# Performance work log

Measured on AMD Instinct MI355X. Metric: run time of the kernel, lower is better.

Reference implementation:

```python
import jax, jax.numpy as jnp
import numpy as np

# dims
E, NB = 16, 4            # encoders, blocks per encoder
B, T = 4, 16             # batch, seq_len
DIN, DM, H = 32, 512, 512  # input dim, block state dim, block hidden
FH = 2048                # per-encoder FFNN hidden
ENC_OUT = 512            # per-encoder output dim
DEC_H, DEC_O, DEC_NH = 2048, 1024, 4  # decoder hidden, output, num hidden layers (num_layers=6 -> in + 4 hidden + out)


def setup_inputs() -> dict:
    key = jax.random.key(0)
    ks = iter(jax.random.split(key, 64))
    s = 0.02
    def p(*shape):
        return jax.random.normal(next(ks), shape, dtype=jnp.float32) * s
    inp = {
        "x": jax.random.normal(next(ks), (B, T, DIN), dtype=jnp.float32),
        # block 0 of each encoder: input = cat[x(32), state(512)] -> 544
        "e0_W0": p(E, DIN + DM, H), "e0_b0": jnp.zeros((E, H), jnp.float32),
        "e0_W1": p(E, H, H),        "e0_b1": jnp.zeros((E, H), jnp.float32),
        "e0_W2": p(E, H, DM),       "e0_b2": jnp.zeros((E, DM), jnp.float32),
        # blocks 1..3: input = cat[prev_state_out(512), state(512)] -> 1024
        "er_W0": p(NB - 1, E, 2 * DM, H), "er_b0": jnp.zeros((NB - 1, E, H), jnp.float32),
        "er_W1": p(NB - 1, E, H, H),      "er_b1": jnp.zeros((NB - 1, E, H), jnp.float32),
        "er_W2": p(NB - 1, E, H, DM),     "er_b2": jnp.zeros((NB - 1, E, DM), jnp.float32),
        # per-encoder FFNN over cat of 4 block states (4*512=2048)
        "ff_W0": p(E, NB * DM, FH), "ff_b0": jnp.zeros((E, FH), jnp.float32),
        "ff_W1": p(E, FH, ENC_OUT), "ff_b1": jnp.zeros((E, ENC_OUT), jnp.float32),
        # decoder recurrent cell: input = cat[16*512, dec_state(1024)] = 9216
        "dec_W0": p(E * ENC_OUT + DEC_O, DEC_H), "dec_b0": jnp.zeros((DEC_H,), jnp.float32),
        "dec_Wh": p(DEC_NH, DEC_H, DEC_H),       "dec_bh": jnp.zeros((DEC_NH, DEC_H), jnp.float32),
        "dec_Wo": p(DEC_H, DEC_O),               "dec_bo": jnp.zeros((DEC_O,), jnp.float32),
    }
    return inp


def reference(x, e0_W0, e0_b0, e0_W1, e0_b1, e0_W2, e0_b2,
              er_W0, er_b0, er_W1, er_b1, er_W2, er_b2,
              ff_W0, ff_b0, ff_W1, ff_b1,
              dec_W0, dec_b0, dec_Wh, dec_bh, dec_Wo, dec_bo):
    Bsz = x.shape[0]

    def elin(z, W, b):  # per-encoder batched linear: (E,B,i) @ (E,i,o)
        return jnp.einsum('ebi,eio->ebo', z, W) + b[:, None, :]

    def step(carry, x_t):
        enc_s, dec_s = carry  # enc_s: (NB,E,B,DM); dec_s: (B,DEC_O)
        xin = jnp.broadcast_to(x_t[None], (E, Bsz, DIN))
        # block 0 cell
        z = jnp.concatenate([xin, enc_s[0]], -1)
        h = jax.nn.gelu(elin(z, e0_W0, e0_b0))
        h = jax.nn.gelu(elin(h, e0_W1, e0_b1))
        s = jnp.tanh(elin(h, e0_W2, e0_b2))
        new_s = [s]
        # blocks 1..3 (fixed small structural loop)
        for r in range(NB - 1):
            z = jnp.concatenate([s, enc_s[r + 1]], -1)
            h = jax.nn.gelu(elin(z, er_W0[r], er_b0[r]))
            h = jax.nn.gelu(elin(h, er_W1[r], er_b1[r]))
            s = jnp.tanh(elin(h, er_W2[r], er_b2[r]))
            new_s.append(s)
        new_enc = jnp.stack(new_s, 0)
        # per-encoder FFNN over concatenated block states
        cat = jnp.concatenate(new_s, -1)  # (E,B,NB*DM)
        out = jax.nn.gelu(elin(cat, ff_W0, ff_b0))
        out = elin(out, ff_W1, ff_b1)     # (E,B,ENC_OUT)
        # decoder recurrent cell over cat of all encoder outputs
        dec_in = jnp.transpose(out, (1, 0, 2)).reshape(Bsz, E * ENC_OUT)
        z = jnp.concatenate([dec_in, dec_s], -1)
        h = jax.nn.gelu(z @ dec_W0 + dec_b0)
        for i in range(DEC_NH):
            h = jax.nn.gelu(h @ dec_Wh[i] + dec_bh[i])
        new_dec = jnp.tanh(h @ dec_Wo + dec_bo)
        return (new_enc, new_dec), new_dec

    enc0 = jnp.zeros((NB, E, Bsz, DM), x.dtype)
    dec0 = jnp.zeros((Bsz, DEC_O), x.dtype)
    _, ys = jax.lax.scan(step, (enc0, dec0), jnp.transpose(x, (1, 0, 2)))
    return jnp.transpose(ys, (1, 0, 2))  # (B,T,DEC_O)
```

## Files before the change

### kernel.cpp

```cpp
#include <hip/hip_runtime.h>
#include <math.h>
#include <stdint.h>

#define AG __HIP_MEMORY_SCOPE_AGENT
typedef unsigned long long ull;

__device__ __forceinline__ float ld4(const float* p) {
  return __hip_atomic_load(p, __ATOMIC_RELAXED, AG);
}
__device__ __forceinline__ void st4(float* p, float v) {
  __hip_atomic_store(p, v, __ATOMIC_RELAXED, AG);
}
__device__ __forceinline__ ull ld8(const float* p) {
  return __hip_atomic_load((const ull*)p, __ATOMIC_RELAXED, AG);
}
__device__ __forceinline__ void fence_vm() {
  asm volatile("s_waitcnt vmcnt(0)" ::: "memory");
}
__device__ __forceinline__ void waitge(unsigned* c, unsigned tgt) {
  if (threadIdx.x == 0) {
    while ((int)(__hip_atomic_load(c, __ATOMIC_RELAXED, AG) - tgt) < 0)
      __builtin_amdgcn_s_sleep(1);
  }
  __syncthreads();
}
__device__ __forceinline__ void wait_epoch(unsigned* line, unsigned epoch) {
  if (threadIdx.x == 0) {
    while ((int)(__hip_atomic_load(line, __ATOMIC_RELAXED, AG) - epoch) < 0)
      __builtin_amdgcn_s_sleep(1);
  }
  __syncthreads();
}
__device__ __forceinline__ void wr2(float* d, ull v) {
  d[0] = __uint_as_float((unsigned)v);
  d[1] = __uint_as_float((unsigned)(v >> 32));
}
__device__ __forceinline__ float act_apply(int act, float v) {
  if (act == 0) {
    float v3 = v * v * v;
    return 0.5f * v * (1.0f + tanhf(0.7978845608028654f * (v + 0.044715f * v3)));
  }
  if (act == 1) return tanhf(v);
  return v;
}

__device__ __forceinline__ void stage_signal(unsigned* stageCnt, unsigned bcT,
                                             unsigned* flag, unsigned epoch,
                                             unsigned* sflag) {
  const int tid = threadIdx.x;
  if (tid == 0) {
    unsigned old = __hip_atomic_fetch_add(stageCnt, 1u, __ATOMIC_RELAXED, AG);
    *sflag = (bcT && old == bcT - 1) ? 1u : 0u;
  }
  __syncthreads();
  if (*sflag) {
    if (tid < 64) __hip_atomic_store(flag + tid * 16, epoch, __ATOMIC_RELAXED, AG);
  }
  __syncthreads();
}

template <int KC, class ZL8, class ST>
__device__ void p4(const float* __restrict__ W, int ldw, const float* __restrict__ bias,
                   int c0, int k0, int chunk, int act, int kc, unsigned kcTgt,
                   unsigned* kcCnt, float* part,
                   unsigned* stageCnt, unsigned bcT, unsigned* flag, unsigned epoch,
                   float* lds, unsigned* sflag, ZL8&& zl8, ST&& store) {
  const int tid = threadIdx.x;
  __syncthreads();
  const int cp = chunk >> 1;
  for (int i = tid; i < 4 * cp; i += 256) {
    int b = i / cp, kp = i - b * cp;
    wr2(&lds[b * chunk + 2 * kp], zl8(b, (k0 >> 1) + kp));
  }
  __syncthreads();
  const int q = tid >> 6, lane = tid & 63;
  const int kg = lane >> 4, j4 = lane & 15;
  const int sub = chunk >> 2;
  const int nk = sub >> 2;
  float acc[4][4];
#pragma unroll
  for (int r = 0; r < 4; ++r)
#pragma unroll
    for (int c = 0; c < 4; ++c) acc[r][c] = 0.f;
  const float* wp = W + (size_t)(k0 + q * sub + kg) * ldw + (c0 + 4 * j4);
  const float* zq = lds + q * sub + kg;
#pragma unroll 16
  for (int kk = 0; kk < nk; ++kk) {
    float4 w4 = *(const float4*)(wp + (size_t)(4 * kk) * ldw);
    float z0 = zq[4 * kk];
    float z1 = zq[chunk + 4 * kk];
    float z2 = zq[2 * chunk + 4 * kk];
    float z3 = zq[3 * chunk + 4 * kk];
    acc[0][0] = fmaf(z0, w4.x, acc[0][0]); acc[0][1] = fmaf(z0, w4.y, acc[0][1]);
    acc[0][2] = fmaf(z0, w4.z, acc[0][2]); acc[0][3] = fmaf(z0, w4.w, acc[0][3]);
    acc[1][0] = fmaf(z1, w4.x, acc[1][0]); acc[1][1] = fmaf(z1, w4.y, acc[1][1]);
    acc[1][2] = fmaf(z1, w4.z, acc[1][2]); acc[1][3] = fmaf(z1, w4.w, acc[1][3]);
    acc[2][0] = fmaf(z2, w4.x, acc[2][0]); acc[2][1] = fmaf(z2, w4.y, acc[2][1]);
    acc[2][2] = fmaf(z2, w4.z, acc[2][2]); acc[2][3] = fmaf(z2, w4.w, acc[2][3]);
    acc[3][0] = fmaf(z3, w4.x, acc[3][0]); acc[3][1] = fmaf(z3, w4.y, acc[3][1]);
    acc[3][2] = fmaf(z3, w4.z, acc[3][2]); acc[3][3] = fmaf(z3, w4.w, acc[3][3]);
  }
  __syncthreads();
  float* red = lds;
  float* myred = red + (q * 4 + kg) * 256 + j4 * 16;
#pragma unroll
  for (int b = 0; b < 4; ++b) {
    float4 v4;
    v4.x = acc[b][0]; v4.y = acc[b][1]; v4.z = acc[b][2]; v4.w = acc[b][3];
    *(float4*)(myred + b * 4) = v4;
  }
  __syncthreads();
  const int j4o = tid >> 4, bb = (tid >> 2) & 3, cc = tid & 3;
  const int oj = 4 * j4o + cc;
  float v = 0.f;
#pragma unroll
  for (int g = 0; g < 16; ++g) v += red[g * 256 + j4o * 16 + bb * 4 + cc];
  if constexpr (KC == 1) {
    if (bias) v += bias[c0 + oj];
    v = act_apply(act, v);
    store(bb, c0 + oj, v);
    fence_vm();
    __syncthreads();
    stage_signal(stageCnt, bcT, flag, epoch, sflag);
  } else {
    st4(&part[kc * 256 + oj * 4 + bb], v);
    fence_vm();
    __syncthreads();
    if (tid == 0) {
      unsigned old = __hip_atomic_fetch_add(kcCnt, 1u, __ATOMIC_RELAXED, AG);
      *sflag = (old == kcTgt - 1) ? 1u : 0u;
    }
    __syncthreads();
    if (*sflag) {
      float s = 0.f;
#pragma unroll
      for (int g = 0; g < KC; ++g) s += ld4(&part[g * 256 + oj * 4 + bb]);
      if (bias) s += bias[c0 + oj];
      s = act_apply(act, s);
      store(bb, c0 + oj, s);
      fence_vm();
      __syncthreads();
      stage_signal(stageCnt, bcT, flag, epoch, sflag);
    }
  }
  __syncthreads();
}

template <int KC, class ZL8, class ST>
__device__ void p64(const float* __restrict__ W, int ldw, const float* __restrict__ bias,
                    int c0, int k0, int k1, int act, int kc, unsigned kcTgt,
                    unsigned* kcCnt, float* part,
                    unsigned* stageCnt, unsigned bcT, unsigned* flag, unsigned epoch,
                    float* lds, unsigned* sflag, ZL8&& zl8, ST&& store) {
  const int tid = threadIdx.x;
  const int tj = tid & 15, tr = tid >> 4;
  float acc[4][4];
#pragma unroll
  for (int r = 0; r < 4; ++r)
#pragma unroll
    for (int c = 0; c < 4; ++c) acc[r][c] = 0.f;
  float* Wl = lds;
  float* Zl = lds + 64 * 68;
  const int wk = tid >> 2, wc = (tid & 3) * 16;
  const int r1 = tid >> 3, c8 = tid & 7;
  for (int kb = k0; kb < k1; kb += 64) {
    __syncthreads();
    {
      const float* src = W + (size_t)(kb + wk) * ldw + c0 + wc;
      float4 w0 = *(const float4*)(src);
      float4 w1 = *(const float4*)(src + 4);
      float4 w2 = *(const float4*)(src + 8);
      float4 w3 = *(const float4*)(src + 12);
      *(float4*)&Wl[wk * 68 + wc + 0]  = w0;
      *(float4*)&Wl[wk * 68 + wc + 4]  = w1;
      *(float4*)&Wl[wk * 68 + wc + 8]  = w2;
      *(float4*)&Wl[wk * 68 + wc + 12] = w3;
    }
    {
      ull v[8];
#pragma unroll
      for (int q = 0; q < 8; ++q) {
        int row = (q < 4) ? r1 : 32 + r1;
        int kp = c8 + 8 * (q & 3);
        v[q] = zl8(row, (kb >> 1) + kp);
      }
#pragma unroll
      for (int q = 0; q < 8; ++q) {
        int row = (q < 4) ? r1 : 32 + r1;
        int kp = c8 + 8 * (q & 3);
        wr2(&Zl[row * 65 + 2 * kp], v[q]);
      }
    }
    __syncthreads();
#pragma unroll 4
    for (int kk = 0; kk < 64; ++kk) {
      float4 w4 = *(float4*)&Wl[kk * 68 + tj * 4];
      float zr0 = Zl[(tr * 4 + 0) * 65 + kk];
      float zr1 = Zl[(tr * 4 + 1) * 65 + kk];
      float zr2 = Zl[(tr * 4 + 2) * 65 + kk];
      float zr3 = Zl[(tr * 4 + 3) * 65 + kk];
      acc[0][0] = fmaf(zr0, w4.x, acc[0][0]); acc[0][1] = fmaf(zr0, w4.y, acc[0][1]);
      acc[0][2] = fmaf(zr0, w4.z, acc[0][2]); acc[0][3] = fmaf(zr0, w4.w, acc[0][3]);
      acc[1][0] = fmaf(zr1, w4.x, acc[1][0]); acc[1][1] = fmaf(zr1, w4.y, acc[1][1]);
      acc[1][2] = fmaf(zr1, w4.z, acc[1][2]); acc[1][3] = fmaf(zr1, w4.w, acc[1][3]);
      acc[2][0] = fmaf(zr2, w4.x, acc[2][0]); acc[2][1] = fmaf(zr2, w4.y, acc[2][1]);
      acc[2][2] = fmaf(zr2, w4.z, acc[2][2]); acc[2][3] = fmaf(zr2, w4.w, acc[2][3]);
      acc[3][0] = fmaf(zr3, w4.x, acc[3][0]); acc[3][1] = fmaf(zr3, w4.y, acc[3][1]);
      acc[3][2] = fmaf(zr3, w4.z, acc[3][2]); acc[3][3] = fmaf(zr3, w4.w, acc[3][3]);
    }
  }
  __syncthreads();
  if constexpr (KC == 1) {
#pragma unroll
    for (int r = 0; r < 4; ++r)
#pragma unroll
      for (int c = 0; c < 4; ++c) {
        int col = c0 + tj * 4 + c;
        float v = acc[r][c] + (bias ? bias[col] : 0.f);
        v = act_apply(act, v);
        store(tr * 4 + r, col, v);
      }
    fence_vm();
    __syncthreads();
    stage_signal(stageCnt, bcT, flag, epoch, sflag);
  } else {
    float* pp = part + kc * 4096;
#pragma unroll
    for (int r = 0; r < 4; ++r)
#pragma unroll
      for (int c = 0; c < 4; ++c)
        st4(&pp[(tr * 4 + r) * 64 + tj * 4 + c], acc[r][c]);
    fence_vm();
    __syncthreads();
    if (tid == 0) {
      unsigned old = __hip_atomic_fetch_add(kcCnt, 1u, __ATOMIC_RELAXED, AG);
      *sflag = (old == kcTgt - 1) ? 1u : 0u;
    }
    __syncthreads();
    if (*sflag) {
      for (int r = 0; r < 4; ++r)
        for (int c = 0; c < 4; ++c) {
          int idx = (tr * 4 + r) * 64 + tj * 4 + c;
          float s = 0.f;
#pragma unroll
          for (int q = 0; q < KC; ++q) s += ld4(&part[q * 4096 + idx]);
          int col = c0 + tj * 4 + c;
          if (bias) s += bias[col];
          s = act_apply(act, s);
          store(tr * 4 + r, col, s);
        }
      fence_vm();
      __syncthreads();
      stage_signal(stageCnt, bcT, flag, epoch, sflag);
    }
  }
  __syncthreads();
}

struct P {
  const float *x;
  const float *e0W0, *e0b0, *e0W1, *e0b1, *e0W2, *e0b2;
  const float *erW0, *erb0, *erW1, *erb1, *erW2, *erb2;
  const float *ffW0, *ffb0, *ffW1, *ffb1;
  const float *dW0, *db0, *dWh, *dbh, *dWo, *dbo;
  float *S, *h1, *h2, *g, *eo, *hd_pre, *hd0, *hd1, *dob, *pF2, *pD;
  unsigned* cnt;
  float* out;
};

#define S_IDX(r, t, e, b) ((size_t)((((r)*16 + (t)) * 16 + (e)) * 4 + (b)) * 512)

#define C_A 0
#define C_B 64
#define C_C 128
#define C_FFG 192
#define C_KF2 208
#define C_FFO 336
#define C_DC 344
#define C_KD 352
#define C_KDO 384
#define C_KL0 400
#define C_L0C 432
#define C_FFLAG 440
#define C_L0FLAG 504
#define C_OFLAG 568
#define C_DFLAG 632

__global__ __launch_bounds__(256, 2) void hrnn(P p) {
  __shared__ __align__(16) float lds[64 * 68 + 64 * 65];
  __shared__ unsigned sflag;
  const int w = blockIdx.x;
  const int e = w & 15, lvl = (w >> 4) & 3, sub = w >> 6;
  auto cptr = [&](int i) { return p.cnt + (size_t)i * 16; };
  unsigned* myline_ff = cptr(C_FFLAG + (w & 63));
  unsigned* myline_l0 = cptr(C_L0FLAG + (w & 63));
  unsigned* myline_out = cptr(C_OFLAG + (w & 63));

  {
    const float *W0, *B0, *W1, *B1, *W2, *B2;
    int K0;
    if (lvl == 0) {
      W0 = p.e0W0 + (size_t)e * 544 * 512; B0 = p.e0b0 + e * 512;
      W1 = p.e0W1 + (size_t)e * 262144;    B1 = p.e0b1 + e * 512;
      W2 = p.e0W2 + (size_t)e * 262144;    B2 = p.e0b2 + e * 512;
      K0 = 544;
    } else {
      int ri = (lvl - 1) * 16 + e;
      W0 = p.erW0 + (size_t)ri * 524288; B0 = p.erb0 + (size_t)ri * 512;
      W1 = p.erW1 + (size_t)ri * 262144; B1 = p.erb1 + (size_t)ri * 512;
      W2 = p.erW2 + (size_t)ri * 262144; B2 = p.erb2 + (size_t)ri * 512;
      K0 = 1024;
    }
    unsigned* aT = cptr(C_A + e * 4 + lvl);
    unsigned* bT = cptr(C_B + e * 4 + lvl);
    unsigned* cT = cptr(C_C + e * 4 + lvl);
    float* h1 = p.h1 + (size_t)(e * 4 + lvl) * 4 * 512;
    float* h2 = p.h2 + (size_t)(e * 4 + lvl) * 4 * 512;
    for (int t = 0; t < 16; ++t) {
      if (t) waitge(cT, 8u * t);
      if (lvl) waitge(cptr(C_C + e * 4 + lvl - 1), 8u * (t + 1));
      {
        const float* x = p.x; const float* S = p.S;
        const int tt = t, ee = e, rr = lvl;
        auto zl = [=](int b, int kp) -> ull {
          if (rr == 0) {
            if (kp < 16) return *(const ull*)(x + ((b * 16 + tt) * 32 + 2 * kp));
            return tt ? ld8(S + S_IDX(0, tt - 1, ee, b) + 2 * kp - 32) : 0ull;
          } else {
            if (kp < 256) return ld8(S + S_IDX(rr - 1, tt, ee, b) + 2 * kp);
            return tt ? ld8(S + S_IDX(rr, tt - 1, ee, b) + 2 * kp - 512) : 0ull;
          }
        };
        auto st = [=](int b, int col, float v) { st4(h1 + b * 512 + col, v); };
        p4<1>(W0, 512, B0, sub * 64, 0, K0, 0, 0, 0, nullptr, nullptr,
              aT, 0, nullptr, 0, lds, &sflag, zl, st);
      }
      waitge(aT, 8u * (t + 1));
      {
        auto zl = [=](int b, int kp) -> ull { return ld8(h1 + b * 512 + 2 * kp); };
        auto st = [=](int b, int col, float v) { st4(h2 + b * 512 + col, v); };
        p4<1>(W1, 512, B1, sub * 64, 0, 512, 0, 0, 0, nullptr, nullptr,
              bT, 0, nullptr, 0, lds, &sflag, zl, st);
      }
      waitge(bT, 8u * (t + 1));
      {
        float* S = p.S; const int tt = t, ee = e, rr = lvl;
        auto zl = [=](int b, int kp) -> ull { return ld8(h2 + b * 512 + 2 * kp); };
        auto st = [=](int b, int col, float v) { st4(S + S_IDX(rr, tt, ee, b) + col, v); };
        p4<1>(W2, 512, B2, sub * 64, 0, 512, 1, 0, 0, nullptr, nullptr,
              cT, 0, nullptr, 0, lds, &sflag, zl, st);
      }
    }
  }

  for (int r = 0; r < 4; ++r) waitge(cptr(C_C + e * 4 + r), 128u);
  {
    const float* S = p.S; const int ee = e;
    auto zl = [=](int row, int kp) -> ull {
      int k = 2 * kp, tt = row >> 2, b = row & 3, seg = k >> 9;
      return ld8(S + S_IDX(seg, tt, ee, b) + (k & 511));
    };
    float* g = p.g + (size_t)e * 131072;
    auto st = [=](int row, int col, float v) { st4(g + (size_t)row * 2048 + col, v); };
    int slot = w >> 4;
    p64<1>(p.ffW0 + (size_t)e * 4194304, 2048, p.ffb0 + e * 2048, slot * 64, 0, 2048,
           0, 0, 0, nullptr, nullptr, cptr(C_FFG + e), 0, nullptr, 0,
           lds, &sflag, zl, st);
  }
  waitge(cptr(C_FFG + e), 32u);
  {
    int ct = w >> 6, kc2 = (w >> 4) & 3;
    const float* g = p.g + (size_t)e * 131072;
    auto zl = [=](int row, int kp) -> ull { return ld8(g + (size_t)row * 2048 + 2 * kp); };
    float* eo = p.eo; const int ee = e;
    auto st = [=](int row, int col, float v) {
      int tt = row >> 2, b = row & 3;
      st4(eo + (size_t)((tt * 16 + ee) * 4 + b) * 512 + col, v);
    };
    p64<4>(p.ffW1 + (size_t)e * 1048576, 512, p.ffb1 + e * 512, ct * 64,
           kc2 * 512, (kc2 + 1) * 512, 2, kc2, 4u,
           cptr(C_KF2 + e * 8 + ct), p.pF2 + (size_t)(e * 8 + ct) * 16384,
           cptr(C_FFO), 128u, cptr(C_FFLAG), 1u, lds, &sflag, zl, st);
  }

  wait_epoch(myline_ff, 1u);
  const int tile = w >> 4, kD = w & 15;
  const int tileO = w >> 5, kO = w & 31;
  {
    const float* eo = p.eo;
    auto zl = [=](int row, int kp) -> ull {
      int k = 2 * kp, tt = row >> 2, b = row & 3, e2 = k >> 9;
      return ld8(eo + (size_t)((tt * 16 + e2) * 4 + b) * 512 + (k & 511));
    };
    float* hp = p.hd_pre;
    auto st = [=](int row, int col, float v) { st4(hp + (size_t)row * 2048 + col, v); };
    p64<16>(p.dW0, 2048, p.db0, tile * 64, kD * 512, (kD + 1) * 512, 2, kD, 16u,
            cptr(C_KL0 + tile), p.pF2 + (size_t)tile * 65536,
            cptr(C_L0C), 32u, cptr(C_L0FLAG), 1u, lds, &sflag, zl, st);
  }
  wait_epoch(myline_l0, 1u);

  {
    const float* dW0b = p.dW0 + (size_t)8192 * 2048;
    for (int t = 0; t < 16; ++t) {
      if (t) wait_epoch(myline_out, (unsigned)t);
      {
        const float* dob = p.dob; const int tt = t;
        auto zl = [=](int b, int kpg) -> ull {
          return tt ? ld8(dob + b * 1024 + 2 * kpg) : 0ull;
        };
        const float* hp = p.hd_pre; float* hd = p.hd0;
        auto st = [=](int b, int col, float v) {
          v += ld4(hp + (size_t)(tt * 4 + b) * 2048 + col);
          v = act_apply(0, v);
          st4(hd + b * 2048 + col, v);
        };
        p4<16>(dW0b, 2048, nullptr, tile * 64, kD * 64, 64, 2, kD, 80u * t + 16u,
               cptr(C_KD + tile), p.pD + (size_t)tile * 4096,
               cptr(C_DC + 0), 32u * (t + 1), cptr(C_DFLAG + 0 * 64), (unsigned)(t + 1),
               lds, &sflag, zl, st);
      }
      for (int l = 1; l <= 4; ++l) {
        wait_epoch(cptr(C_DFLAG + (l - 1) * 64 + (w & 63)), (unsigned)(t + 1));
        const float* hin = (l & 1) ? p.hd0 : p.hd1;
        float* hout = (l & 1) ? p.hd1 : p.hd0;
        auto zl = [=](int b, int kp) -> ull { return ld8(hin + b * 2048 + 2 * kp); };
        auto st = [=](int b, int col, float v) { st4(hout + b * 2048 + col, v); };
        p4<16>(p.dWh + (size_t)(l - 1) * 4194304, 2048, p.dbh + (size_t)(l - 1) * 2048,
               tile * 64, kD * 128, 128, 0, kD, 80u * t + 16u * (l + 1),
               cptr(C_KD + tile), p.pD + (size_t)tile * 4096,
               cptr(C_DC + l), 32u * (t + 1), cptr(C_DFLAG + l * 64), (unsigned)(t + 1),
               lds, &sflag, zl, st);
      }
      wait_epoch(cptr(C_DFLAG + 4 * 64 + (w & 63)), (unsigned)(t + 1));
      {
        const float* hin = p.hd0; float* dob = p.dob; float* outp = p.out; const int tt = t;
        auto zl = [=](int b, int kp) -> ull { return ld8(hin + b * 2048 + 2 * kp); };
        auto st = [=](int b, int col, float v) {
          outp[(size_t)(b * 16 + tt) * 1024 + col] = v;
          st4(dob + b * 1024 + col, v);
        };
        p4<32>(p.dWo, 1024, p.dbo, tileO * 64, kO * 64, 64, 1, kO, 32u * (t + 1),
               cptr(C_KDO + tileO), p.pD + (size_t)tileO * 8192,
               cptr(C_DC + 5), 16u * (t + 1), cptr(C_OFLAG), (unsigned)(t + 1),
               lds, &sflag, zl, st);
      }
    }
  }
}

extern "C" void kernel_launch(void* const* d_in, const int* in_sizes, int n_in,
                              void* d_out, int out_size, void* d_ws, size_t ws_size,
                              hipStream_t stream) {
  hipMemsetAsync(d_ws, 0, 65536, stream);

  P p;
  p.x    = (const float*)d_in[0];
  p.e0W0 = (const float*)d_in[1];  p.e0b0 = (const float*)d_in[2];
  p.e0W1 = (const float*)d_in[3];  p.e0b1 = (const float*)d_in[4];
  p.e0W2 = (const float*)d_in[5];  p.e0b2 = (const float*)d_in[6];
  p.erW0 = (const float*)d_in[7];  p.erb0 = (const float*)d_in[8];
  p.erW1 = (const float*)d_in[9];  p.erb1 = (const float*)d_in[10];
  p.erW2 = (const float*)d_in[11]; p.erb2 = (const float*)d_in[12];
  p.ffW0 = (const float*)d_in[13]; p.ffb0 = (const float*)d_in[14];
  p.ffW1 = (const float*)d_in[15]; p.ffb1 = (const float*)d_in[16];
  p.dW0  = (const float*)d_in[17]; p.db0  = (const float*)d_in[18];
  p.dWh  = (const float*)d_in[19]; p.dbh  = (const float*)d_in[20];
  p.dWo  = (const float*)d_in[21]; p.dbo  = (const float*)d_in[22];

  float* base = (float*)((char*)d_ws + 65536);
  p.S      = base; base += 2097152;
  p.h1     = base; base += 131072;
  p.h2     = base; base += 131072;
  p.g      = base; base += 2097152;
  p.eo     = base; base += 524288;
  p.hd_pre = base; base += 131072;
  p.hd0    = base; base += 8192;
  p.hd1    = base; base += 8192;
  p.dob    = base; base += 4096;
  p.pF2    = base; base += 2097152;
  p.pD     = base; base += 131072;

  p.cnt = (unsigned*)d_ws;
  p.out = (float*)d_out;

  hipLaunchKernelGGL(hrnn, dim3(512), dim3(256), 0, stream, p);
}
```

Before: 1.995 ms.

## Double persistent grid to 1024 blocks and split-K all stages across more workgroups

Launches 1024 persistent workgroups instead of 512, with launch bounds raised to four blocks per CU. Encoder blocks now handle 32 columns each through a new specialized GEMV routine (p4e) that splits K across 32 thread groups and reduces through LDS. The FFNN, decoder layer-0 and decoder hidden stages use twice as many K-splits with enlarged partial buffers and counters. The aim is to spread the latency-bound recurrent GEMVs over more CUs and waves, at the cost of more partial-sum traffic and more atomic synchronization, and the dense grid depends on all 1024 blocks being co-resident.

```diff
diff --git a/kernel.cpp b/kernel.cpp
--- a/kernel.cpp
+++ b/kernel.cpp
@@ -56,6 +56,68 @@
   if (*sflag) {
     if (tid < 64) __hip_atomic_store(flag + tid * 16, epoch, __ATOMIC_RELAXED, AG);
   }
+  __syncthreads();
+}
+
+template <class ZL8, class ST>
+__device__ void p4e(const float* __restrict__ W, const float* __restrict__ bias,
+                    int c0, int chunk, int act, unsigned* stageCnt,
+                    float* lds, ZL8&& zl8, ST&& store) {
+  const int tid = threadIdx.x;
+  __syncthreads();
+  const int cp = chunk >> 1;
+  for (int i = tid; i < 4 * cp; i += 256) {
+    int b = i / cp, kp = i - b * cp;
+    wr2(&lds[b * chunk + 2 * kp], zl8(b, kp));
+  }
+  __syncthreads();
+  const int g = tid >> 3, j4 = tid & 7;
+  const int sub = chunk >> 5;
+  float acc[4][4];
+#pragma unroll
+  for (int r = 0; r < 4; ++r)
+#pragma unroll
+    for (int c = 0; c < 4; ++c) acc[r][c] = 0.f;
+  const float* wp = W + (size_t)(g * sub) * 512 + c0 + 4 * j4;
+  const float* zq = lds + g * sub;
+#pragma unroll 8
+  for (int kk = 0; kk < sub; ++kk) {
+    float4 w4 = *(const float4*)(wp + (size_t)kk * 512);
+    float z0 = zq[kk];
+    float z1 = zq[chunk + kk];
+    float z2 = zq[2 * chunk + kk];
+    float z3 = zq[3 * chunk + kk];
+    acc[0][0] = fmaf(z0, w4.x, acc[0][0]); acc[0][1] = fmaf(z0, w4.y, acc[0][1]);
+    acc[0][2] = fmaf(z0, w4.z, acc[0][2]); acc[0][3] = fmaf(z0, w4.w, acc[0][3]);
+    acc[1][0] = fmaf(z1, w4.x, acc[1][0]); acc[1][1] = fmaf(z1, w4.y, acc[1][1]);
+    acc[1][2] = fmaf(z1, w4.z, acc[1][2]); acc[1][3] = fmaf(z1, w4.w, acc[1][3]);
+    acc[2][0] = fmaf(z2, w4.x, acc[2][0]); acc[2][1] = fmaf(z2, w4.y, acc[2][1]);
+    acc[2][2] = fmaf(z2, w4.z, acc[2][2]); acc[2][3] = fmaf(z2, w4.w, acc[2][3]);
+    acc[3][0] = fmaf(z3, w4.x, acc[3][0]); acc[3][1] = fmaf(z3, w4.y, acc[3][1]);
+    acc[3][2] = fmaf(z3, w4.z, acc[3][2]); acc[3][3] = fmaf(z3, w4.w, acc[3][3]);
+  }
+  float* red = lds + 4096;
+  float* myred = red + g * 128 + j4 * 16;
+#pragma unroll
+  for (int b = 0; b < 4; ++b) {
+    float4 v4;
+    v4.x = acc[b][0]; v4.y = acc[b][1]; v4.z = acc[b][2]; v4.w = acc[b][3];
+    *(float4*)(myred + b * 4) = v4;
+  }
+  __syncthreads();
+  if (tid < 128) {
+    const int o = tid;
+    float v = 0.f;
+#pragma unroll
+    for (int gg = 0; gg < 32; ++gg) v += red[gg * 128 + o];
+    const int col = c0 + 4 * (o >> 4) + (o & 3), b = (o >> 2) & 3;
+    if (bias) v += bias[col];
+    v = act_apply(act, v);
+    store(b, col, v);
+  }
+  fence_vm();
+  __syncthreads();
+  if (tid == 0) __hip_atomic_fetch_add(stageCnt, 1u, __ATOMIC_RELAXED, AG);
   __syncthreads();
 }
 
@@ -263,7 +325,7 @@
   const float *erW0, *erb0, *erW1, *erb1, *erW2, *erb2;
   const float *ffW0, *ffb0, *ffW1, *ffb1;
   const float *dW0, *db0, *dWh, *dbh, *dWo, *dbo;
-  float *S, *h1, *h2, *g, *eo, *hd_pre, *hd0, *hd1, *dob, *pF2, *pD;
+  float *S, *h1, *h2, *g, *eo, *hd_pre, *hd0, *hd1, *dob, *pBig, *pD;
   unsigned* cnt;
   float* out;
 };
@@ -274,29 +336,32 @@
 #define C_B 64
 #define C_C 128
 #define C_FFG 192
-#define C_KF2 208
-#define C_FFO 336
-#define C_DC 344
-#define C_KD 352
-#define C_KDO 384
-#define C_KL0 400
-#define C_L0C 432
-#define C_FFLAG 440
-#define C_L0FLAG 504
-#define C_OFLAG 568
-#define C_DFLAG 632
-
-__global__ __launch_bounds__(256, 2) void hrnn(P p) {
+#define C_KF1 208
+#define C_KF2 720
+#define C_FFO 848
+#define C_DC 856
+#define C_KD 864
+#define C_KDO 896
+#define C_KL0 912
+#define C_L0C 944
+#define C_FFLAG 952
+#define C_L0FLAG 1016
+#define C_OFLAG 1080
+#define C_DFLAG 1144
+
+__global__ __launch_bounds__(256, 4) void hrnn(P p) {
   __shared__ __align__(16) float lds[64 * 68 + 64 * 65];
   __shared__ unsigned sflag;
   const int w = blockIdx.x;
-  const int e = w & 15, lvl = (w >> 4) & 3, sub = w >> 6;
+  const int e = w & 15;
   auto cptr = [&](int i) { return p.cnt + (size_t)i * 16; };
   unsigned* myline_ff = cptr(C_FFLAG + (w & 63));
   unsigned* myline_l0 = cptr(C_L0FLAG + (w & 63));
   unsigned* myline_out = cptr(C_OFLAG + (w & 63));
 
   {
+    const int lvl = (w >> 4) & 3, s32 = w >> 6;
+    const int c0e = s32 * 32;
     const float *W0, *B0, *W1, *B1, *W2, *B2;
     int K0;
     if (lvl == 0) {
@@ -314,11 +379,11 @@
     unsigned* aT = cptr(C_A + e * 4 + lvl);
     unsigned* bT = cptr(C_B + e * 4 + lvl);
     unsigned* cT = cptr(C_C + e * 4 + lvl);
-    float* h1 = p.h1 + (size_t)(e * 4 + lvl) * 4 * 512;
-    float* h2 = p.h2 + (size_t)(e * 4 + lvl) * 4 * 512;
+    float* h1 = p.h1 + (size_t)(e * 4 + lvl) * 2048;
+    float* h2 = p.h2 + (size_t)(e * 4 + lvl) * 2048;
     for (int t = 0; t < 16; ++t) {
-      if (t) waitge(cT, 8u * t);
-      if (lvl) waitge(cptr(C_C + e * 4 + lvl - 1), 8u * (t + 1));
+      if (t) waitge(cT, 16u * t);
+      if (lvl) waitge(cptr(C_C + e * 4 + lvl - 1), 16u * (t + 1));
       {
         const float* x = p.x; const float* S = p.S;
         const int tt = t, ee = e, rr = lvl;
@@ -332,28 +397,26 @@
           }
         };
         auto st = [=](int b, int col, float v) { st4(h1 + b * 512 + col, v); };
-        p4<1>(W0, 512, B0, sub * 64, 0, K0, 0, 0, 0, nullptr, nullptr,
-              aT, 0, nullptr, 0, lds, &sflag, zl, st);
-      }
-      waitge(aT, 8u * (t + 1));
+        p4e(W0, B0, c0e, K0, 0, aT, lds, zl, st);
+      }
+      waitge(aT, 16u * (t + 1));
       {
         auto zl = [=](int b, int kp) -> ull { return ld8(h1 + b * 512 + 2 * kp); };
         auto st = [=](int b, int col, float v) { st4(h2 + b * 512 + col, v); };
-        p4<1>(W1, 512, B1, sub * 64, 0, 512, 0, 0, 0, nullptr, nullptr,
-              bT, 0, nullptr, 0, lds, &sflag, zl, st);
-      }
-      waitge(bT, 8u * (t + 1));
+        p4e(W1, B1, c0e, 512, 0, bT, lds, zl, st);
+      }
+      waitge(bT, 16u * (t + 1));
       {
         float* S = p.S; const int tt = t, ee = e, rr = lvl;
         auto zl = [=](int b, int kp) -> ull { return ld8(h2 + b * 512 + 2 * kp); };
         auto st = [=](int b, int col, float v) { st4(S + S_IDX(rr, tt, ee, b) + col, v); };
-        p4<1>(W2, 512, B2, sub * 64, 0, 512, 1, 0, 0, nullptr, nullptr,
-              cT, 0, nullptr, 0, lds, &sflag, zl, st);
-      }
-    }
-  }
-
-  for (int r = 0; r < 4; ++r) waitge(cptr(C_C + e * 4 + r), 128u);
+        p4e(W2, B2, c0e, 512, 1, cT, lds, zl, st);
+      }
+    }
+  }
+
+  for (int r = 0; r < 4; ++r) waitge(cptr(C_C + e * 4 + r), 256u);
+  const int r6 = w >> 4;
   {
     const float* S = p.S; const int ee = e;
     auto zl = [=](int row, int kp) -> ull {
@@ -362,14 +425,15 @@
     };
     float* g = p.g + (size_t)e * 131072;
     auto st = [=](int row, int col, float v) { st4(g + (size_t)row * 2048 + col, v); };
-    int slot = w >> 4;
-    p64<1>(p.ffW0 + (size_t)e * 4194304, 2048, p.ffb0 + e * 2048, slot * 64, 0, 2048,
-           0, 0, 0, nullptr, nullptr, cptr(C_FFG + e), 0, nullptr, 0,
-           lds, &sflag, zl, st);
+    int ct = r6 & 31, kc = r6 >> 5;
+    p64<2>(p.ffW0 + (size_t)e * 4194304, 2048, p.ffb0 + e * 2048, ct * 64,
+           kc * 1024, (kc + 1) * 1024, 0, kc, 2u,
+           cptr(C_KF1 + e * 32 + ct), p.pBig + (size_t)e * 262144 + ct * 8192,
+           cptr(C_FFG + e), 0, nullptr, 0, lds, &sflag, zl, st);
   }
   waitge(cptr(C_FFG + e), 32u);
   {
-    int ct = w >> 6, kc2 = (w >> 4) & 3;
+    int ct2 = r6 & 7, kc2 = r6 >> 3;
     const float* g = p.g + (size_t)e * 131072;
     auto zl = [=](int row, int kp) -> ull { return ld8(g + (size_t)row * 2048 + 2 * kp); };
     float* eo = p.eo; const int ee = e;
@@ -377,15 +441,14 @@
       int tt = row >> 2, b = row & 3;
       st4(eo + (size_t)((tt * 16 + ee) * 4 + b) * 512 + col, v);
     };
-    p64<4>(p.ffW1 + (size_t)e * 1048576, 512, p.ffb1 + e * 512, ct * 64,
-           kc2 * 512, (kc2 + 1) * 512, 2, kc2, 4u,
-           cptr(C_KF2 + e * 8 + ct), p.pF2 + (size_t)(e * 8 + ct) * 16384,
+    p64<8>(p.ffW1 + (size_t)e * 1048576, 512, p.ffb1 + e * 512, ct2 * 64,
+           kc2 * 256, (kc2 + 1) * 256, 2, kc2, 8u,
+           cptr(C_KF2 + e * 8 + ct2), p.pBig + (size_t)e * 262144 + ct2 * 32768,
            cptr(C_FFO), 128u, cptr(C_FFLAG), 1u, lds, &sflag, zl, st);
   }
 
   wait_epoch(myline_ff, 1u);
-  const int tile = w >> 4, kD = w & 15;
-  const int tileO = w >> 5, kO = w & 31;
+  const int tile = w & 31, kc32 = w >> 5;
   {
     const float* eo = p.eo;
     auto zl = [=](int row, int kp) -> ull {
@@ -394,14 +457,15 @@
     };
     float* hp = p.hd_pre;
     auto st = [=](int row, int col, float v) { st4(hp + (size_t)row * 2048 + col, v); };
-    p64<16>(p.dW0, 2048, p.db0, tile * 64, kD * 512, (kD + 1) * 512, 2, kD, 16u,
-            cptr(C_KL0 + tile), p.pF2 + (size_t)tile * 65536,
+    p64<32>(p.dW0, 2048, p.db0, tile * 64, kc32 * 256, (kc32 + 1) * 256, 2, kc32, 32u,
+            cptr(C_KL0 + tile), p.pBig + (size_t)tile * 131072,
             cptr(C_L0C), 32u, cptr(C_L0FLAG), 1u, lds, &sflag, zl, st);
   }
   wait_epoch(myline_l0, 1u);
 
   {
     const float* dW0b = p.dW0 + (size_t)8192 * 2048;
+    const int tileO = (w >> 5) & 15, kO = w & 31;
     for (int t = 0; t < 16; ++t) {
       if (t) wait_epoch(myline_out, (unsigned)t);
       {
@@ -415,8 +479,8 @@
           v = act_apply(0, v);
           st4(hd + b * 2048 + col, v);
         };
-        p4<16>(dW0b, 2048, nullptr, tile * 64, kD * 64, 64, 2, kD, 80u * t + 16u,
-               cptr(C_KD + tile), p.pD + (size_t)tile * 4096,
+        p4<32>(dW0b, 2048, nullptr, tile * 64, kc32 * 32, 32, 2, kc32, 160u * t + 32u,
+               cptr(C_KD + tile), p.pD + (size_t)tile * 8192,
                cptr(C_DC + 0), 32u * (t + 1), cptr(C_DFLAG + 0 * 64), (unsigned)(t + 1),
                lds, &sflag, zl, st);
       }
@@ -426,14 +490,14 @@
         float* hout = (l & 1) ? p.hd1 : p.hd0;
         auto zl = [=](int b, int kp) -> ull { return ld8(hin + b * 2048 + 2 * kp); };
         auto st = [=](int b, int col, float v) { st4(hout + b * 2048 + col, v); };
-        p4<16>(p.dWh + (size_t)(l - 1) * 4194304, 2048, p.dbh + (size_t)(l - 1) * 2048,
-               tile * 64, kD * 128, 128, 0, kD, 80u * t + 16u * (l + 1),
-               cptr(C_KD + tile), p.pD + (size_t)tile * 4096,
+        p4<32>(p.dWh + (size_t)(l - 1) * 4194304, 2048, p.dbh + (size_t)(l - 1) * 2048,
+               tile * 64, kc32 * 64, 64, 0, kc32, 160u * t + 32u * (l + 1),
+               cptr(C_KD + tile), p.pD + (size_t)tile * 8192,
                cptr(C_DC + l), 32u * (t + 1), cptr(C_DFLAG + l * 64), (unsigned)(t + 1),
                lds, &sflag, zl, st);
       }
       wait_epoch(cptr(C_DFLAG + 4 * 64 + (w & 63)), (unsigned)(t + 1));
-      {
+      if (w < 512) {
         const float* hin = p.hd0; float* dob = p.dob; float* outp = p.out; const int tt = t;
         auto zl = [=](int b, int kp) -> ull { return ld8(hin + b * 2048 + 2 * kp); };
         auto st = [=](int b, int col, float v) {
@@ -441,7 +505,7 @@
           st4(dob + b * 1024 + col, v);
         };
         p4<32>(p.dWo, 1024, p.dbo, tileO * 64, kO * 64, 64, 1, kO, 32u * (t + 1),
-               cptr(C_KDO + tileO), p.pD + (size_t)tileO * 8192,
+               cptr(C_KDO + tileO), p.pD + 262144 + (size_t)tileO * 8192,
                cptr(C_DC + 5), 16u * (t + 1), cptr(C_OFLAG), (unsigned)(t + 1),
                lds, &sflag, zl, st);
       }
@@ -452,7 +516,7 @@
 extern "C" void kernel_launch(void* const* d_in, const int* in_sizes, int n_in,
                               void* d_out, int out_size, void* d_ws, size_t ws_size,
                               hipStream_t stream) {
-  hipMemsetAsync(d_ws, 0, 65536, stream);
+  hipMemsetAsync(d_ws, 0, 131072, stream);
 
   P p;
   p.x    = (const float*)d_in[0];
@@ -468,7 +532,7 @@
   p.dWh  = (const float*)d_in[19]; p.dbh  = (const float*)d_in[20];
   p.dWo  = (const float*)d_in[21]; p.dbo  = (const float*)d_in[22];
 
-  float* base = (float*)((char*)d_ws + 65536);
+  float* base = (float*)((char*)d_ws + 131072);
   p.S      = base; base += 2097152;
   p.h1     = base; base += 131072;
   p.h2     = base; base += 131072;
@@ -478,11 +542,10 @@
   p.hd0    = base; base += 8192;
   p.hd1    = base; base += 8192;
   p.dob    = base; base += 4096;
-  p.pF2    = base; base += 2097152;
-  p.pD     = base; base += 131072;
-
+  p.pBig   = base; base += 4194304;
+  p.pD     = base; base += 393216;
   p.cnt = (unsigned*)d_ws;
   p.out = (float*)d_out;
 
-  hipLaunchKernelGGL(hrnn, dim3(512), dim3(256), 0, stream, p);
-}
+  hipLaunchKernelGGL(hrnn, dim3(1024), dim3(256), 0, stream, p);
+}
```

New measurement: 2.548 ms. 1.28x slower.

## Split encoder recurrence across 1024 blocks with 32-column tiles and new matvec

Applied to the files above, without the earlier changes.

The launch grows from 512 to 1024 workgroups. Each encoder block's linear layers are now split into 16 column slices of 32 instead of 8 slices of 64. A new specialized matvec routine with compile-time K chunking and an LDS tree reduction replaces the generic p4 in the recurrent phase, and the stage counters are retargeted to 16 arrivals. Occupancy is raised to 4 blocks per CU with smaller LDS so the extra workgroups stay co-resident. Blocks beyond 512 exit after the recurrence, which halves per-block weight streaming on the serial critical path but adds more atomic sync traffic.

```diff
diff --git a/kernel.cpp b/kernel.cpp
--- a/kernel.cpp
+++ b/kernel.cpp
@@ -56,6 +56,71 @@
   if (*sflag) {
     if (tid < 64) __hip_atomic_store(flag + tid * 16, epoch, __ATOMIC_RELAXED, AG);
   }
+  __syncthreads();
+}
+
+template <int CHUNK, class ZL8, class ST>
+__device__ void p4e32(const float* __restrict__ W, const float* __restrict__ bias,
+                      int c0, int act, unsigned* stageCnt,
+                      float* lds, ZL8&& zl8, ST&& store) {
+  const int tid = threadIdx.x;
+  __syncthreads();
+  constexpr int CP = CHUNK >> 1;
+  for (int i = tid; i < 4 * CP; i += 256) {
+    int b = i / CP, kp = i - b * CP;
+    wr2(&lds[b * CHUNK + 2 * kp], zl8(b, kp));
+  }
+  __syncthreads();
+  const int q = tid >> 6, lane = tid & 63;
+  const int kg = lane >> 3, j4 = lane & 7;
+  constexpr int SUB = CHUNK >> 2;
+  constexpr int KS = SUB >> 3;
+  float acc[4][4];
+#pragma unroll
+  for (int r = 0; r < 4; ++r)
+#pragma unroll
+    for (int c = 0; c < 4; ++c) acc[r][c] = 0.f;
+  const float* wp = W + (size_t)(q * SUB + kg * KS) * 512 + c0 + 4 * j4;
+  const float* zq = lds + q * SUB + kg * KS;
+#pragma unroll 16
+  for (int kk = 0; kk < KS; ++kk) {
+    float4 w4 = *(const float4*)(wp + (size_t)kk * 512);
+    float z0 = zq[kk];
+    float z1 = zq[CHUNK + kk];
+    float z2 = zq[2 * CHUNK + kk];
+    float z3 = zq[3 * CHUNK + kk];
+    acc[0][0] = fmaf(z0, w4.x, acc[0][0]); acc[0][1] = fmaf(z0, w4.y, acc[0][1]);
+    acc[0][2] = fmaf(z0, w4.z, acc[0][2]); acc[0][3] = fmaf(z0, w4.w, acc[0][3]);
+    acc[1][0] = fmaf(z1, w4.x, acc[1][0]); acc[1][1] = fmaf(z1, w4.y, acc[1][1]);
+    acc[1][2] = fmaf(z1, w4.z, acc[1][2]); acc[1][3] = fmaf(z1, w4.w, acc[1][3]);
+    acc[2][0] = fmaf(z2, w4.x, acc[2][0]); acc[2][1] = fmaf(z2, w4.y, acc[2][1]);
+    acc[2][2] = fmaf(z2, w4.z, acc[2][2]); acc[2][3] = fmaf(z2, w4.w, acc[2][3]);
+    acc[3][0] = fmaf(z3, w4.x, acc[3][0]); acc[3][1] = fmaf(z3, w4.y, acc[3][1]);
+    acc[3][2] = fmaf(z3, w4.z, acc[3][2]); acc[3][3] = fmaf(z3, w4.w, acc[3][3]);
+  }
+  __syncthreads();
+  float* red = lds;
+  float* myred = red + (q * 8 + kg) * 128 + j4 * 16;
+#pragma unroll
+  for (int b = 0; b < 4; ++b) {
+    float4 v4;
+    v4.x = acc[b][0]; v4.y = acc[b][1]; v4.z = acc[b][2]; v4.w = acc[b][3];
+    *(float4*)(myred + b * 4) = v4;
+  }
+  __syncthreads();
+  if (tid < 128) {
+    const int o = tid;
+    float v = 0.f;
+#pragma unroll
+    for (int g = 0; g < 32; ++g) v += red[g * 128 + o];
+    const int col = c0 + 4 * (o >> 4) + (o & 3), b = (o >> 2) & 3;
+    v += bias[col];
+    v = act_apply(act, v);
+    store(b, col, v);
+  }
+  fence_vm();
+  __syncthreads();
+  if (tid == 0) __hip_atomic_fetch_add(stageCnt, 1u, __ATOMIC_RELAXED, AG);
   __syncthreads();
 }
 
@@ -286,30 +351,25 @@
 #define C_OFLAG 568
 #define C_DFLAG 632
 
-__global__ __launch_bounds__(256, 2) void hrnn(P p) {
-  __shared__ __align__(16) float lds[64 * 68 + 64 * 65];
+__global__ __launch_bounds__(256, 4) void hrnn(P p) {
+  __shared__ __align__(16) float lds[8512];
   __shared__ unsigned sflag;
   const int w = blockIdx.x;
-  const int e = w & 15, lvl = (w >> 4) & 3, sub = w >> 6;
+  const int e = w & 15, lvl = (w >> 4) & 3, cs16 = w >> 6;
   auto cptr = [&](int i) { return p.cnt + (size_t)i * 16; };
-  unsigned* myline_ff = cptr(C_FFLAG + (w & 63));
-  unsigned* myline_l0 = cptr(C_L0FLAG + (w & 63));
-  unsigned* myline_out = cptr(C_OFLAG + (w & 63));
 
   {
+    const int c0e = cs16 * 32;
     const float *W0, *B0, *W1, *B1, *W2, *B2;
-    int K0;
     if (lvl == 0) {
       W0 = p.e0W0 + (size_t)e * 544 * 512; B0 = p.e0b0 + e * 512;
       W1 = p.e0W1 + (size_t)e * 262144;    B1 = p.e0b1 + e * 512;
       W2 = p.e0W2 + (size_t)e * 262144;    B2 = p.e0b2 + e * 512;
-      K0 = 544;
     } else {
       int ri = (lvl - 1) * 16 + e;
       W0 = p.erW0 + (size_t)ri * 524288; B0 = p.erb0 + (size_t)ri * 512;
       W1 = p.erW1 + (size_t)ri * 262144; B1 = p.erb1 + (size_t)ri * 512;
       W2 = p.erW2 + (size_t)ri * 262144; B2 = p.erb2 + (size_t)ri * 512;
-      K0 = 1024;
     }
     unsigned* aT = cptr(C_A + e * 4 + lvl);
     unsigned* bT = cptr(C_B + e * 4 + lvl);
@@ -317,43 +377,49 @@
     float* h1 = p.h1 + (size_t)(e * 4 + lvl) * 4 * 512;
     float* h2 = p.h2 + (size_t)(e * 4 + lvl) * 4 * 512;
     for (int t = 0; t < 16; ++t) {
-      if (t) waitge(cT, 8u * t);
-      if (lvl) waitge(cptr(C_C + e * 4 + lvl - 1), 8u * (t + 1));
+      if (t) waitge(cT, 16u * t);
+      if (lvl) waitge(cptr(C_C + e * 4 + lvl - 1), 16u * (t + 1));
       {
         const float* x = p.x; const float* S = p.S;
         const int tt = t, ee = e, rr = lvl;
-        auto zl = [=](int b, int kp) -> ull {
-          if (rr == 0) {
+        auto st = [=](int b, int col, float v) { st4(h1 + b * 512 + col, v); };
+        if (rr == 0) {
+          auto zl = [=](int b, int kp) -> ull {
             if (kp < 16) return *(const ull*)(x + ((b * 16 + tt) * 32 + 2 * kp));
             return tt ? ld8(S + S_IDX(0, tt - 1, ee, b) + 2 * kp - 32) : 0ull;
-          } else {
+          };
+          p4e32<544>(W0, B0, c0e, 0, aT, lds, zl, st);
+        } else {
+          auto zl = [=](int b, int kp) -> ull {
             if (kp < 256) return ld8(S + S_IDX(rr - 1, tt, ee, b) + 2 * kp);
             return tt ? ld8(S + S_IDX(rr, tt - 1, ee, b) + 2 * kp - 512) : 0ull;
-          }
-        };
-        auto st = [=](int b, int col, float v) { st4(h1 + b * 512 + col, v); };
-        p4<1>(W0, 512, B0, sub * 64, 0, K0, 0, 0, 0, nullptr, nullptr,
-              aT, 0, nullptr, 0, lds, &sflag, zl, st);
-      }
-      waitge(aT, 8u * (t + 1));
+          };
+          p4e32<1024>(W0, B0, c0e, 0, aT, lds, zl, st);
+        }
+      }
+      waitge(aT, 16u * (t + 1));
       {
         auto zl = [=](int b, int kp) -> ull { return ld8(h1 + b * 512 + 2 * kp); };
         auto st = [=](int b, int col, float v) { st4(h2 + b * 512 + col, v); };
-        p4<1>(W1, 512, B1, sub * 64, 0, 512, 0, 0, 0, nullptr, nullptr,
-              bT, 0, nullptr, 0, lds, &sflag, zl, st);
-      }
-      waitge(bT, 8u * (t + 1));
+        p4e32<512>(W1, B1, c0e, 0, bT, lds, zl, st);
+      }
+      waitge(bT, 16u * (t + 1));
       {
         float* S = p.S; const int tt = t, ee = e, rr = lvl;
         auto zl = [=](int b, int kp) -> ull { return ld8(h2 + b * 512 + 2 * kp); };
         auto st = [=](int b, int col, float v) { st4(S + S_IDX(rr, tt, ee, b) + col, v); };
-        p4<1>(W2, 512, B2, sub * 64, 0, 512, 1, 0, 0, nullptr, nullptr,
-              cT, 0, nullptr, 0, lds, &sflag, zl, st);
-      }
-    }
-  }
-
-  for (int r = 0; r < 4; ++r) waitge(cptr(C_C + e * 4 + r), 128u);
+        p4e32<512>(W2, B2, c0e, 1, cT, lds, zl, st);
+      }
+    }
+  }
+
+  if (w >= 512) return;
+
+  unsigned* myline_ff = cptr(C_FFLAG + (w & 63));
+  unsigned* myline_l0 = cptr(C_L0FLAG + (w & 63));
+  unsigned* myline_out = cptr(C_OFLAG + (w & 63));
+
+  for (int r = 0; r < 4; ++r) waitge(cptr(C_C + e * 4 + r), 256u);
   {
     const float* S = p.S; const int ee = e;
     auto zl = [=](int row, int kp) -> ull {
@@ -484,5 +550,5 @@
   p.cnt = (unsigned*)d_ws;
   p.out = (float*)d_out;
 
-  hipLaunchKernelGGL(hrnn, dim3(512), dim3(256), 0, stream, p);
-}
+  hipLaunchKernelGGL(hrnn, dim3(1024), dim3(256), 0, stream, p);
+}
```

After: 2.569 ms. 28.8% more time.
